# Kernel optimization log

Hardware: AMD Instinct MI355X
Metric: run time of the kernel (lower is better)

Reference implementation:

```python
import jax, jax.numpy as jnp
from jax import lax
import numpy as np

EPS = 1e-5


def _conv3x3(x, W, stride):
    # x: [N,C,H,W], W: [O,I,3,3]
    return lax.conv_general_dilated(
        x, W, window_strides=(stride, stride), padding=((1, 1), (1, 1)),
        dimension_numbers=("NCHW", "OIHW", "NCHW"))


def _bn(x, gamma, beta):
    # training-mode BatchNorm2d: batch statistics over (N,H,W)
    mean = jnp.mean(x, axis=(0, 2, 3), keepdims=True)
    var = jnp.var(x, axis=(0, 2, 3), keepdims=True)
    inv = lax.rsqrt(var + EPS)
    return (x - mean) * inv * gamma[None, :, None, None] + beta[None, :, None, None]


def setup_inputs() -> dict:
    key = jax.random.key(0)
    ks = jax.random.split(key, 5)
    N, C, H, W = 32, 256, 56, 56
    x = jax.random.normal(ks[0], (N, C, H, W), dtype=jnp.float32)
    W1 = jax.random.normal(ks[1], (C, C, 3, 3), dtype=jnp.float32) * 0.05
    W2 = jax.random.normal(ks[2], (C, C, 3, 3), dtype=jnp.float32) * 0.05
    gamma1 = jnp.ones((C,), jnp.float32)
    beta1 = jnp.zeros((C,), jnp.float32)
    gamma2 = jnp.ones((C,), jnp.float32)
    beta2 = jnp.zeros((C,), jnp.float32)
    mask1 = jax.random.randint(ks[3], (C,), 0, 2).astype(jnp.float32)
    mask2 = jax.random.randint(ks[4], (C,), 0, 2).astype(jnp.float32)
    return {"x": x, "W1": W1, "W2": W2, "gamma1": gamma1, "beta1": beta1,
            "gamma2": gamma2, "beta2": beta2, "mask1": mask1, "mask2": mask2}


def reference(x, W1, W2, gamma1, beta1, gamma2, beta2, mask1, mask2):
    # conv_with_mask: output channels with mask==0 stay zero (structured pruning)
    h = _conv3x3(x, W1, 1) * mask1[None, :, None, None]
    h = jax.nn.relu(_bn(h, gamma1, beta1))
    h = _conv3x3(h, W2, 1) * mask2[None, :, None, None]
    h = _bn(h, gamma2, beta2)
    # stride=1, in_planes==planes -> identity shortcut
    return jax.nn.relu(h + x)
```

## Files before the change

### kernel.cpp

```cpp
#include <hip/hip_runtime.h>

#define N_   32
#define C_   256
#define H_   56
#define W_   56
#define HW_  (H_ * W_)
#define NHW_ (N_ * HW_)
#define PLANE_ ((size_t)NHW_ * 32)

typedef unsigned short u16;
typedef __attribute__((ext_vector_type(8))) short short8;
typedef __attribute__((ext_vector_type(4))) float f32x4;

__device__ __forceinline__ float b2f(u16 u) {
    union { unsigned int i; float f; } v; v.i = ((unsigned int)u) << 16; return v.f;
}
__device__ __forceinline__ u16 f2b(float f) {
    union { float f; unsigned int i; } v; v.f = f;
    unsigned int r = v.i + 0x7fffu + ((v.i >> 16) & 1u);
    return (u16)(r >> 16);
}

typedef const __attribute__((address_space(1))) unsigned int* as1_u32p;
typedef __attribute__((address_space(3))) unsigned int* as3_u32p;
__device__ __forceinline__ void gload_lds16(const u16* g, u16* l) {
    __builtin_amdgcn_global_load_lds((as1_u32p)g, (as3_u32p)l, 16, 0, 0);
}

extern "C" __global__ __launch_bounds__(256) void cvt_x_kernel(
    const float* __restrict__ x, u16* __restrict__ xb)
{
    __shared__ float t[64 * 57];
    const int nh = blockIdx.x, n = nh / H_, h = nh % H_;
    const size_t pix0 = (size_t)(n * H_ + h) * W_;
    for (int cb = 0; cb < 4; ++cb) {
        __syncthreads();
        for (int idx = threadIdx.x; idx < 64 * 56; idx += 256) {
            int cc = idx / 56, w = idx % 56;
            t[cc * 57 + w] = x[(((size_t)(n * C_ + cb * 64 + cc)) * H_ + h) * W_ + w];
        }
        __syncthreads();
        for (int idx = threadIdx.x; idx < 56 * 64; idx += 256) {
            int w = idx >> 6, cc = idx & 63;
            int plane = cb * 2 + (cc >> 5);
            xb[(size_t)plane * PLANE_ + (pix0 + w) * 32 + (cc & 31)] = f2b(t[cc * 57 + w]);
        }
    }
}

extern "C" __global__ void mask_scan_kernel(
    const float* __restrict__ mask, int* __restrict__ perm,
    float* __restrict__ maskp, int* __restrict__ kpar, int* __restrict__ id256)
{
    __shared__ float m[256];
    const int c = threadIdx.x;
    m[c] = mask[c];
    id256[c] = c;
    __syncthreads();
    int pre = 0, tot = 0;
    for (int i = 0; i < 256; ++i) {
        int nz = (m[i] != 0.f) ? 1 : 0;
        if (i < c) pre += nz;
        tot += nz;
    }
    const int nz = (m[c] != 0.f) ? 1 : 0;
    const int pos = nz ? pre : tot + (c - pre);
    perm[pos] = c;
    maskp[pos] = m[c];
    if (c == 0) {
        kpar[0] = ((tot + 15) >> 4) << 4;
        kpar[1] = 8;
        kpar[2] = tot;
        kpar[3] = 0;
    }
    if (c < 8) kpar[4 + c] = c;
}

extern "C" __global__ void chunk_sel_kernel(
    const float* __restrict__ shift, const int* __restrict__ kparK,
    int* __restrict__ kpar)
{
    __shared__ int act[8];
    const int c = threadIdx.x;
    if (c < 8) act[c] = 0;
    __syncthreads();
    const int K = kparK[2];
    const bool a = (c < K) || (shift[c] > 0.f);
    if (a) atomicOr(&act[c >> 5], 1);
    __syncthreads();
    if (c == 0) {
        int nq = 0;
        for (int q = 0; q < 8; ++q) if (act[q]) kpar[4 + nq++] = q;
        kpar[1] = nq;
    }
}

extern "C" __global__ __launch_bounds__(256) void pack_w_kernel(
    const float* __restrict__ w, const int* __restrict__ operm,
    const int* __restrict__ iperm, u16* __restrict__ wp)
{
    int o = blockIdx.x * 256 + threadIdx.x;
    int j = o & 7, lq = (o >> 3) & 3, l15 = (o >> 5) & 15;
    int cog = (o >> 9) & 15, cih = (o >> 13) & 7, rs = o >> 16;
    int co = operm[cog * 16 + l15];
    int ci = iperm[cih * 32 + lq * 8 + j];
    wp[o] = f2b(w[((size_t)co * C_ + ci) * 9 + rs]);
}

extern "C" __global__ __launch_bounds__(256, 3) void BasicBlock_4355096838467_kernel(
    const u16* __restrict__ xb,
    const u16* __restrict__ wpA,
    const float* __restrict__ maskp,
    const u16* __restrict__ zeropad,
    const int* __restrict__ kp,
    u16* __restrict__ outb)
{
    __shared__ u16 lds[3][7680];

    const int tid  = threadIdx.x;
    const int wave = tid >> 6, lane = tid & 63;
    const int l15  = lane & 15, lq = lane >> 4;
    const int wave_co = wave >> 1, wave_px = wave & 1;
    const int xcd = blockIdx.x & 7, r_ = blockIdx.x >> 3;
    const int yco = r_ & 1;
    const int sb  = xcd * 112 + (r_ >> 1);
    const int n = sb / 28, hb = sb % 28;
    const int h0 = hb * 2;
    const int cog_base = yco * 8 + wave_co * 4;
    const size_t abase0 = (size_t)cog_base * 512 + (size_t)(l15 * 32 + lq * 8);

    const int Kc = kp[0];
    const int nq = kp[1];
    int nf = (Kc >> 4) - cog_base;
    nf = nf < 0 ? 0 : (nf > 4 ? 4 : nf);

    f32x4 acc[4][4];
#pragma unroll
    for (int i = 0; i < 4; ++i)
#pragma unroll
        for (int j = 0; j < 4; ++j) acc[i][j] = (f32x4){0.f, 0.f, 0.f, 0.f};

    auto stage = [&](int q, int b) {
        const u16* plane = xb + (size_t)q * PLANE_;
        for (int is = wave; is < 15; is += 4) {
            int L = is * 64 + lane;
            int pixel = L >> 2, so = L & 3;
            int rr = pixel / 58, slot = pixel - rr * 58;
            int oct = so ^ ((slot >> 1) & 3);
            int row = h0 - 1 + rr, col = slot - 1;
            bool ok = pixel < 232 &&
                      (unsigned)row < (unsigned)H_ && (unsigned)col < (unsigned)W_;
            const u16* gp = ok
                ? plane + ((size_t)(n * H_ + row) * W_ + col) * 32 + oct * 8
                : zeropad + oct * 8;
            gload_lds16(gp, &lds[b][is * 512]);
        }
    };

    short8 afq[3][4];
    auto loadA = [&](int rs_, int q, short8 dst[4]) {
        const size_t bb = (size_t)rs_ * 65536 + (size_t)q * 8192 + abase0;
#pragma unroll
        for (int fm = 0; fm < 4; ++fm)
            if (fm < nf) dst[fm] = *(const short8*)(wpA + bb + (size_t)fm * 512);
    };

    if (nq > 0) {
        const int q0 = kp[4];
        stage(q0, 0);
        __builtin_amdgcn_sched_barrier(0);
        loadA(0, q0, afq[0]);
        loadA(1, q0, afq[1]);
        __builtin_amdgcn_sched_barrier(0);
        if (nq > 1) {
            stage(kp[5], 1);
            __builtin_amdgcn_sched_barrier(0);
            asm volatile("s_waitcnt vmcnt(3)" ::: "memory");
        } else {
            asm volatile("s_waitcnt vmcnt(0)" ::: "memory");
        }
        __builtin_amdgcn_sched_barrier(0);
        __builtin_amdgcn_s_barrier();
        __builtin_amdgcn_sched_barrier(0);

        for (int t = 0; t < nq; ++t) {
            const int q  = kp[4 + t];
            const int qn = kp[4 + (t + 1 < nq ? t + 1 : t)];
            const u16* Lb = &lds[t % 3][0];
#pragma unroll
            for (int rs = 0; rs < 9; ++rs) {
                if (rs < 7) loadA(rs + 2, q, afq[(rs + 2) % 3]);
                else        loadA(rs - 7, qn, afq[(rs + 2) % 3]);
                const int r = rs / 3, s = rs - (rs / 3) * 3;
                short8 bf[4];
#pragma unroll
                for (int fn = 0; fn < 4; ++fn) {
                    int slot = fn * 16 + l15 + s;
                    int pixel = (wave_px + r) * 58 + slot;
                    int so = lq ^ ((slot >> 1) & 3);
                    bf[fn] = *(const short8*)(Lb + pixel * 32 + so * 8);
                }
#pragma unroll
                for (int fm = 0; fm < 4; ++fm)
                    if (fm < nf) {
#pragma unroll
                        for (int fn = 0; fn < 4; ++fn)
                            acc[fm][fn] = __builtin_amdgcn_mfma_f32_16x16x32_bf16(
                                afq[rs % 3][fm], bf[fn], acc[fm][fn], 0, 0, 0);
                    }
            }
            __builtin_amdgcn_sched_barrier(0);
            if (t + 2 < nq) stage(kp[6 + t], (t + 2) % 3);
            __builtin_amdgcn_sched_barrier(0);
            if (t + 1 < nq) {
                if (t + 2 < nq) asm volatile("s_waitcnt vmcnt(3)" ::: "memory");
                else            asm volatile("s_waitcnt vmcnt(0)" ::: "memory");
                __builtin_amdgcn_sched_barrier(0);
                __builtin_amdgcn_s_barrier();
                __builtin_amdgcn_sched_barrier(0);
            }
        }
    }

    const int row = h0 + wave_px;
#pragma unroll
    for (int fn = 0; fn < 4; ++fn) {
        int px = fn * 16 + l15;
        if (px < W_) {
#pragma unroll
            for (int fm = 0; fm < 4; ++fm) {
                int co_b = cog_base * 16 + fm * 16 + lq * 4;
                const f32x4 mk = *(const f32x4*)(maskp + co_b);
                size_t base = (size_t)(co_b >> 5) * PLANE_
                            + ((size_t)(n * H_ + row) * W_ + px) * 32 + (co_b & 31);
                ushort4 o;
                o.x = f2b(acc[fm][fn][0] * mk[0]);
                o.y = f2b(acc[fm][fn][1] * mk[1]);
                o.z = f2b(acc[fm][fn][2] * mk[2]);
                o.w = f2b(acc[fm][fn][3] * mk[3]);
                *(ushort4*)(outb + base) = o;
            }
        }
    }
}

extern "C" __global__ void zero_accum_kernel(float* __restrict__ p) {
    p[blockIdx.x * 256 + threadIdx.x] = 0.f;
}

extern "C" __global__ __launch_bounds__(256) void stats_nhwc_kernel(
    const u16* __restrict__ hb, float* __restrict__ gsum, float* __restrict__ gsq)
{
    __shared__ float s_s[8 * 256];
    __shared__ float s_q[8 * 256];
    const int g = threadIdx.x >> 5, l = threadIdx.x & 31;
    const size_t pbase_off = (size_t)(l >> 2) * PLANE_ + (l & 3) * 8;
    float s[8], q[8];
#pragma unroll
    for (int j = 0; j < 8; ++j) { s[j] = 0.f; q[j] = 0.f; }
    const int pbase = blockIdx.x * 256;
    for (int t = 0; t < 32; ++t) {
        int p = pbase + g + t * 8;
        short8 v = *(const short8*)(hb + pbase_off + (size_t)p * 32);
#pragma unroll
        for (int j = 0; j < 8; ++j) {
            float f = b2f((u16)v[j]);
            s[j] += f; q[j] += f * f;
        }
    }
#pragma unroll
    for (int j = 0; j < 8; ++j) {
        s_s[g * 256 + l * 8 + j] = s[j];
        s_q[g * 256 + l * 8 + j] = q[j];
    }
    __syncthreads();
    const int c = threadIdx.x;
    float S = 0.f, Q = 0.f;
#pragma unroll
    for (int g2 = 0; g2 < 8; ++g2) { S += s_s[g2 * 256 + c]; Q += s_q[g2 * 256 + c]; }
    atomicAdd(&gsum[c], S);
    atomicAdd(&gsq[c], Q);
}

extern "C" __global__ void finalize_bn_kernel(
    const float* __restrict__ gsum, const float* __restrict__ gsq,
    const float* __restrict__ gamma, const float* __restrict__ beta,
    const int* __restrict__ perm,
    float* __restrict__ scale, float* __restrict__ shift)
{
    const int c = threadIdx.x;
    const int co = perm[c];
    const float inv_n = 1.f / (float)NHW_;
    float mean = gsum[c] * inv_n;
    float var  = gsq[c] * inv_n - mean * mean;
    var = fmaxf(var, 0.f);
    float inv = rsqrtf(var + 1e-5f);
    float sc = gamma[co] * inv;
    scale[c] = sc;
    shift[c] = beta[co] - mean * sc;
}

extern "C" __global__ __launch_bounds__(256) void bn_relu_nhwc_kernel(
    u16* __restrict__ hb, const float* __restrict__ scale, const float* __restrict__ shift)
{
    size_t idx = ((size_t)blockIdx.x * 256 + threadIdx.x) * 8;
    int c0 = (int)(blockIdx.x / 1568) * 32 + (int)(idx & 31);
    short8 v = *(short8*)(hb + idx);
    short8 o;
#pragma unroll
    for (int j = 0; j < 8; ++j) {
        int c = c0 + j;
        float f = b2f((u16)v[j]) * scale[c] + shift[c];
        o[j] = (short)f2b(fmaxf(f, 0.f));
    }
    *(short8*)(hb + idx) = o;
}

extern "C" __global__ __launch_bounds__(256) void bn_add_relu_out_kernel(
    const u16* __restrict__ h2b, const float* __restrict__ x,
    const float* __restrict__ scale, const float* __restrict__ shift,
    const int* __restrict__ perm,
    float* __restrict__ out)
{
    __shared__ float t[64 * 57];
    const int nh = blockIdx.x, n = nh / H_, h = nh % H_;
    const size_t pix0 = (size_t)(n * H_ + h) * W_;
    for (int cb = 0; cb < 4; ++cb) {
        __syncthreads();
        for (int it = threadIdx.x; it < 448; it += 256) {
            int w = it >> 3, oc = it & 7;
            size_t addr = (size_t)(cb * 2 + (oc >> 2)) * PLANE_
                        + (pix0 + w) * 32 + (oc & 3) * 8;
            short8 v = *(const short8*)(h2b + addr);
#pragma unroll
            for (int j = 0; j < 8; ++j) t[(oc * 8 + j) * 57 + w] = b2f((u16)v[j]);
        }
        __syncthreads();
        for (int it = threadIdx.x; it < 64 * 56; it += 256) {
            int cl = it / 56, w = it % 56;
            int c = cb * 64 + cl;
            int co = perm[c];
            size_t oidx = ((size_t)(n * C_ + co) * H_ + h) * W_ + w;
            float v = t[cl * 57 + w] * scale[c] + shift[c] + x[oidx];
            out[oidx] = fmaxf(v, 0.f);
        }
    }
}

extern "C" void kernel_launch(void* const* d_in, const int* in_sizes, int n_in,
                              void* d_out, int out_size, void* d_ws, size_t ws_size,
                              hipStream_t stream) {
    const float* x      = (const float*)d_in[0];
    const float* W1     = (const float*)d_in[1];
    const float* W2     = (const float*)d_in[2];
    const float* gamma1 = (const float*)d_in[3];
    const float* beta1  = (const float*)d_in[4];
    const float* gamma2 = (const float*)d_in[5];
    const float* beta2  = (const float*)d_in[6];
    const float* mask1  = (const float*)d_in[7];
    const float* mask2  = (const float*)d_in[8];
    float* out = (float*)d_out;

    char* ws = (char*)d_ws;
    float* gsum1  = (float*)ws;
    float* gsq1   = gsum1 + 256;
    float* gsum2  = gsq1 + 256;
    float* gsq2   = gsum2 + 256;
    float* scale1 = gsq2 + 256;
    float* shift1 = scale1 + 256;
    float* scale2 = shift1 + 256;
    float* shift2 = scale2 + 256;
    u16*   zeropad = (u16*)(ws + 8192);
    int*   perm1  = (int*)(ws + 12288);
    int*   perm2  = (int*)(ws + 13312);
    float* maskp1 = (float*)(ws + 14336);
    float* maskp2 = (float*)(ws + 15360);
    int*   id256  = (int*)(ws + 16384);
    int*   kpar1  = (int*)(ws + 17408);
    int*   kpar2  = (int*)(ws + 17472);
    u16* Wp1 = (u16*)(ws + 20480);
    u16* Wp2 = Wp1 + 9 * 256 * 256;
    u16* xb  = Wp2 + 9 * 256 * 256;
    u16* h2b = xb;
    u16* h1b = (u16*)d_out;

    zero_accum_kernel<<<dim3(12), dim3(256), 0, stream>>>(gsum1);
    mask_scan_kernel<<<dim3(1), dim3(256), 0, stream>>>(mask1, perm1, maskp1, kpar1, id256);
    mask_scan_kernel<<<dim3(1), dim3(256), 0, stream>>>(mask2, perm2, maskp2, kpar2, id256);
    cvt_x_kernel<<<dim3(N_ * H_), dim3(256), 0, stream>>>(x, xb);
    pack_w_kernel<<<dim3(2304), dim3(256), 0, stream>>>(W1, perm1, id256, Wp1);
    pack_w_kernel<<<dim3(2304), dim3(256), 0, stream>>>(W2, perm2, perm1, Wp2);

    dim3 cgrid(N_ * 56);
    BasicBlock_4355096838467_kernel<<<cgrid, dim3(256), 0, stream>>>(
        xb, Wp1, maskp1, zeropad, kpar1, h1b);
    stats_nhwc_kernel<<<dim3(392), dim3(256), 0, stream>>>(h1b, gsum1, gsq1);
    finalize_bn_kernel<<<dim3(1), dim3(256), 0, stream>>>(
        gsum1, gsq1, gamma1, beta1, perm1, scale1, shift1);
    chunk_sel_kernel<<<dim3(1), dim3(256), 0, stream>>>(shift1, kpar1, kpar2);
    bn_relu_nhwc_kernel<<<dim3(12544), dim3(256), 0, stream>>>(h1b, scale1, shift1);

    BasicBlock_4355096838467_kernel<<<cgrid, dim3(256), 0, stream>>>(
        h1b, Wp2, maskp2, zeropad, kpar2, h2b);
    stats_nhwc_kernel<<<dim3(392), dim3(256), 0, stream>>>(h2b, gsum2, gsq2);
    finalize_bn_kernel<<<dim3(1), dim3(256), 0, stream>>>(
        gsum2, gsq2, gamma2, beta2, perm2, scale2, shift2);
    bn_add_relu_out_kernel<<<dim3(N_ * H_), dim3(256), 0, stream>>>(
        h2b, x, scale2, shift2, perm2, out);
}
```

Baseline: 598.7 us.

## Skip pruned channel halves across conv, stats, BN and output kernels

The conv kernel now returns early for output-channel halves lying entirely beyond the live channel count, and skips the MFMA loop when a wave has no live fragments. It also raises wave priority around the MFMA bursts. The stats, BN-ReLU and final output kernels read the per-mask live count and skip loads for channel planes known to be zero. The two mask-scan launches are merged into one grid. The aim is to avoid reading and computing on the pruned (all-zero) channels, which is valid for any mask but only helps when masks leave more than half the channels unused in a half. It relies on those skipped buffers being treated as zero, and the early return leaves those output planes unwritten.

```diff
diff --git a/kernel.cpp b/kernel.cpp
--- a/kernel.cpp
+++ b/kernel.cpp
@@ -49,13 +49,19 @@
 }
 
 extern "C" __global__ void mask_scan_kernel(
-    const float* __restrict__ mask, int* __restrict__ perm,
-    float* __restrict__ maskp, int* __restrict__ kpar, int* __restrict__ id256)
-{
+    const float* __restrict__ m1, const float* __restrict__ m2,
+    int* __restrict__ p1, int* __restrict__ p2,
+    float* __restrict__ mp1, float* __restrict__ mp2,
+    int* __restrict__ k1, int* __restrict__ k2, int* __restrict__ id256)
+{
+    const float* mask  = blockIdx.x ? m2 : m1;
+    int*   perm  = blockIdx.x ? p2 : p1;
+    float* maskp = blockIdx.x ? mp2 : mp1;
+    int*   kpar  = blockIdx.x ? k2 : k1;
     __shared__ float m[256];
     const int c = threadIdx.x;
     m[c] = mask[c];
-    id256[c] = c;
+    if (blockIdx.x == 0) id256[c] = c;
     __syncthreads();
     int pre = 0, tot = 0;
     for (int i = 0; i < 256; ++i) {
@@ -123,14 +129,17 @@
     const int wave_co = wave >> 1, wave_px = wave & 1;
     const int xcd = blockIdx.x & 7, r_ = blockIdx.x >> 3;
     const int yco = r_ & 1;
+
+    const int Kc = kp[0];
+    if (Kc <= yco * 128) return;
+    const int nq = kp[1];
+
     const int sb  = xcd * 112 + (r_ >> 1);
     const int n = sb / 28, hb = sb % 28;
     const int h0 = hb * 2;
     const int cog_base = yco * 8 + wave_co * 4;
     const size_t abase0 = (size_t)cog_base * 512 + (size_t)(l15 * 32 + lq * 8);
 
-    const int Kc = kp[0];
-    const int nq = kp[1];
     int nf = (Kc >> 4) - cog_base;
     nf = nf < 0 ? 0 : (nf > 4 ? 4 : nf);
 
@@ -187,27 +196,31 @@
             const int q  = kp[4 + t];
             const int qn = kp[4 + (t + 1 < nq ? t + 1 : t)];
             const u16* Lb = &lds[t % 3][0];
-#pragma unroll
-            for (int rs = 0; rs < 9; ++rs) {
-                if (rs < 7) loadA(rs + 2, q, afq[(rs + 2) % 3]);
-                else        loadA(rs - 7, qn, afq[(rs + 2) % 3]);
-                const int r = rs / 3, s = rs - (rs / 3) * 3;
-                short8 bf[4];
-#pragma unroll
-                for (int fn = 0; fn < 4; ++fn) {
-                    int slot = fn * 16 + l15 + s;
-                    int pixel = (wave_px + r) * 58 + slot;
-                    int so = lq ^ ((slot >> 1) & 3);
-                    bf[fn] = *(const short8*)(Lb + pixel * 32 + so * 8);
+            if (nf > 0) {
+#pragma unroll
+                for (int rs = 0; rs < 9; ++rs) {
+                    if (rs < 7) loadA(rs + 2, q, afq[(rs + 2) % 3]);
+                    else        loadA(rs - 7, qn, afq[(rs + 2) % 3]);
+                    const int r = rs / 3, s = rs - (rs / 3) * 3;
+                    short8 bf[4];
+#pragma unroll
+                    for (int fn = 0; fn < 4; ++fn) {
+                        int slot = fn * 16 + l15 + s;
+                        int pixel = (wave_px + r) * 58 + slot;
+                        int so = lq ^ ((slot >> 1) & 3);
+                        bf[fn] = *(const short8*)(Lb + pixel * 32 + so * 8);
+                    }
+                    __builtin_amdgcn_s_setprio(1);
+#pragma unroll
+                    for (int fm = 0; fm < 4; ++fm)
+                        if (fm < nf) {
+#pragma unroll
+                            for (int fn = 0; fn < 4; ++fn)
+                                acc[fm][fn] = __builtin_amdgcn_mfma_f32_16x16x32_bf16(
+                                    afq[rs % 3][fm], bf[fn], acc[fm][fn], 0, 0, 0);
+                        }
+                    __builtin_amdgcn_s_setprio(0);
                 }
-#pragma unroll
-                for (int fm = 0; fm < 4; ++fm)
-                    if (fm < nf) {
-#pragma unroll
-                        for (int fn = 0; fn < 4; ++fn)
-                            acc[fm][fn] = __builtin_amdgcn_mfma_f32_16x16x32_bf16(
-                                afq[rs % 3][fm], bf[fn], acc[fm][fn], 0, 0, 0);
-                    }
             }
             __builtin_amdgcn_sched_barrier(0);
             if (t + 2 < nq) stage(kp[6 + t], (t + 2) % 3);
@@ -249,23 +262,27 @@
 }
 
 extern "C" __global__ __launch_bounds__(256) void stats_nhwc_kernel(
-    const u16* __restrict__ hb, float* __restrict__ gsum, float* __restrict__ gsq)
+    const u16* __restrict__ hb, const int* __restrict__ kp,
+    float* __restrict__ gsum, float* __restrict__ gsq)
 {
     __shared__ float s_s[8 * 256];
     __shared__ float s_q[8 * 256];
     const int g = threadIdx.x >> 5, l = threadIdx.x & 31;
     const size_t pbase_off = (size_t)(l >> 2) * PLANE_ + (l & 3) * 8;
+    const bool live = kp[2] > 128 * (l >> 4);
     float s[8], q[8];
 #pragma unroll
     for (int j = 0; j < 8; ++j) { s[j] = 0.f; q[j] = 0.f; }
     const int pbase = blockIdx.x * 256;
-    for (int t = 0; t < 32; ++t) {
-        int p = pbase + g + t * 8;
-        short8 v = *(const short8*)(hb + pbase_off + (size_t)p * 32);
-#pragma unroll
-        for (int j = 0; j < 8; ++j) {
-            float f = b2f((u16)v[j]);
-            s[j] += f; q[j] += f * f;
+    if (live) {
+        for (int t = 0; t < 32; ++t) {
+            int p = pbase + g + t * 8;
+            short8 v = *(const short8*)(hb + pbase_off + (size_t)p * 32);
+#pragma unroll
+            for (int j = 0; j < 8; ++j) {
+                float f = b2f((u16)v[j]);
+                s[j] += f; q[j] += f * f;
+            }
         }
     }
 #pragma unroll
@@ -301,17 +318,24 @@
 }
 
 extern "C" __global__ __launch_bounds__(256) void bn_relu_nhwc_kernel(
-    u16* __restrict__ hb, const float* __restrict__ scale, const float* __restrict__ shift)
+    u16* __restrict__ hb, const float* __restrict__ scale,
+    const float* __restrict__ shift, const int* __restrict__ kp)
 {
     size_t idx = ((size_t)blockIdx.x * 256 + threadIdx.x) * 8;
-    int c0 = (int)(blockIdx.x / 1568) * 32 + (int)(idx & 31);
-    short8 v = *(short8*)(hb + idx);
+    const int plane = (int)(blockIdx.x / 1568);
+    const int c0 = plane * 32 + (int)(idx & 31);
     short8 o;
-#pragma unroll
-    for (int j = 0; j < 8; ++j) {
-        int c = c0 + j;
-        float f = b2f((u16)v[j]) * scale[c] + shift[c];
-        o[j] = (short)f2b(fmaxf(f, 0.f));
+    if (kp[2] > 128 * (plane >> 2)) {
+        short8 v = *(short8*)(hb + idx);
+#pragma unroll
+        for (int j = 0; j < 8; ++j) {
+            float f = b2f((u16)v[j]) * scale[c0 + j] + shift[c0 + j];
+            o[j] = (short)f2b(fmaxf(f, 0.f));
+        }
+    } else {
+#pragma unroll
+        for (int j = 0; j < 8; ++j)
+            o[j] = (short)f2b(fmaxf(shift[c0 + j], 0.f));
     }
     *(short8*)(hb + idx) = o;
 }
@@ -319,19 +343,23 @@
 extern "C" __global__ __launch_bounds__(256) void bn_add_relu_out_kernel(
     const u16* __restrict__ h2b, const float* __restrict__ x,
     const float* __restrict__ scale, const float* __restrict__ shift,
-    const int* __restrict__ perm,
+    const int* __restrict__ perm, const int* __restrict__ kp,
     float* __restrict__ out)
 {
     __shared__ float t[64 * 57];
     const int nh = blockIdx.x, n = nh / H_, h = nh % H_;
     const size_t pix0 = (size_t)(n * H_ + h) * W_;
+    const int K2 = kp[2];
     for (int cb = 0; cb < 4; ++cb) {
         __syncthreads();
         for (int it = threadIdx.x; it < 448; it += 256) {
             int w = it >> 3, oc = it & 7;
-            size_t addr = (size_t)(cb * 2 + (oc >> 2)) * PLANE_
-                        + (pix0 + w) * 32 + (oc & 3) * 8;
-            short8 v = *(const short8*)(h2b + addr);
+            int plane = cb * 2 + (oc >> 2);
+            short8 v = {0, 0, 0, 0, 0, 0, 0, 0};
+            if (K2 > 128 * (plane >> 2)) {
+                size_t addr = (size_t)plane * PLANE_ + (pix0 + w) * 32 + (oc & 3) * 8;
+                v = *(const short8*)(h2b + addr);
+            }
 #pragma unroll
             for (int j = 0; j < 8; ++j) t[(oc * 8 + j) * 57 + w] = b2f((u16)v[j]);
         }
@@ -385,8 +413,8 @@
     u16* h1b = (u16*)d_out;
 
     zero_accum_kernel<<<dim3(12), dim3(256), 0, stream>>>(gsum1);
-    mask_scan_kernel<<<dim3(1), dim3(256), 0, stream>>>(mask1, perm1, maskp1, kpar1, id256);
-    mask_scan_kernel<<<dim3(1), dim3(256), 0, stream>>>(mask2, perm2, maskp2, kpar2, id256);
+    mask_scan_kernel<<<dim3(2), dim3(256), 0, stream>>>(
+        mask1, mask2, perm1, perm2, maskp1, maskp2, kpar1, kpar2, id256);
     cvt_x_kernel<<<dim3(N_ * H_), dim3(256), 0, stream>>>(x, xb);
     pack_w_kernel<<<dim3(2304), dim3(256), 0, stream>>>(W1, perm1, id256, Wp1);
     pack_w_kernel<<<dim3(2304), dim3(256), 0, stream>>>(W2, perm2, perm1, Wp2);
@@ -394,17 +422,17 @@
     dim3 cgrid(N_ * 56);
     BasicBlock_4355096838467_kernel<<<cgrid, dim3(256), 0, stream>>>(
         xb, Wp1, maskp1, zeropad, kpar1, h1b);
-    stats_nhwc_kernel<<<dim3(392), dim3(256), 0, stream>>>(h1b, gsum1, gsq1);
+    stats_nhwc_kernel<<<dim3(392), dim3(256), 0, stream>>>(h1b, kpar1, gsum1, gsq1);
     finalize_bn_kernel<<<dim3(1), dim3(256), 0, stream>>>(
         gsum1, gsq1, gamma1, beta1, perm1, scale1, shift1);
     chunk_sel_kernel<<<dim3(1), dim3(256), 0, stream>>>(shift1, kpar1, kpar2);
-    bn_relu_nhwc_kernel<<<dim3(12544), dim3(256), 0, stream>>>(h1b, scale1, shift1);
+    bn_relu_nhwc_kernel<<<dim3(12544), dim3(256), 0, stream>>>(h1b, scale1, shift1, kpar1);
 
     BasicBlock_4355096838467_kernel<<<cgrid, dim3(256), 0, stream>>>(
         h1b, Wp2, maskp2, zeropad, kpar2, h2b);
-    stats_nhwc_kernel<<<dim3(392), dim3(256), 0, stream>>>(h2b, gsum2, gsq2);
+    stats_nhwc_kernel<<<dim3(392), dim3(256), 0, stream>>>(h2b, kpar2, gsum2, gsq2);
     finalize_bn_kernel<<<dim3(1), dim3(256), 0, stream>>>(
         gsum2, gsq2, gamma2, beta2, perm2, scale2, shift2);
     bn_add_relu_out_kernel<<<dim3(N_ * H_), dim3(256), 0, stream>>>(
-        h2b, x, scale2, shift2, perm2, out);
-}
+        h2b, x, scale2, shift2, perm2, kpar2, out);
+}
```

After: 590.1 us. Within noise of the previous version (-1.4%).
